# Kernel optimization log

Measured on AMD Instinct MI355X. Metric: run time of the kernel, lower is better.

Reference implementation:

```python
import jax, jax.numpy as jnp
import numpy as np

D_MODEL = 1024
N_HEADS = 16
HEAD_DIM = D_MODEL // N_HEADS
B, S = 2, 2048


def setup_inputs() -> dict:
    key = jax.random.key(0)
    ks = jax.random.split(key, 6)
    w_scale = 1.0 / np.sqrt(D_MODEL)
    return {
        "query": jax.random.normal(ks[0], (B, S, D_MODEL), dtype=jnp.float32),
        "Wq": jax.random.normal(ks[1], (D_MODEL, D_MODEL), dtype=jnp.float32) * w_scale,
        "Wk": jax.random.normal(ks[2], (D_MODEL, D_MODEL), dtype=jnp.float32) * w_scale,
        "Wv": jax.random.normal(ks[3], (D_MODEL, D_MODEL), dtype=jnp.float32) * w_scale,
        "Wo": jax.random.normal(ks[4], (D_MODEL, D_MODEL), dtype=jnp.float32) * w_scale,
        "bo": jnp.zeros((D_MODEL,), dtype=jnp.float32),
    }


def reference(query, Wq, Wk, Wv, Wo, bo):
    # Self-attention: key = value = query (forward() defaults).
    b, t, _ = query.shape
    # Q/K/V projections (nn.Linear applies x @ W.T; weights here are stored as
    # [out, in] like torch, so project with W.T). Split into heads: [B,H,T,Dh].
    def proj(x, W):
        return (x @ W.T).reshape(b, t, N_HEADS, HEAD_DIM).transpose(0, 2, 1, 3)

    q = proj(query, Wq)
    k = proj(query, Wk)
    v = proj(query, Wv)

    scale = 1.0 / np.sqrt(HEAD_DIM)
    scores = jnp.einsum("bhqd,bhkd->bhqk", q, k) * scale  # [B,H,T,T]
    # Causal mask (is_causal=True, not cross-attention).
    causal = jnp.tril(jnp.ones((t, t), dtype=bool))
    scores = jnp.where(causal, scores, jnp.finfo(scores.dtype).min)
    weights = jax.nn.softmax(scores, axis=-1)
    out = jnp.einsum("bhqk,bhkd->bhqd", weights, v)  # [B,H,T,Dh]
    out = out.transpose(0, 2, 1, 3).reshape(b, t, D_MODEL)
    # Output projection with bias (dropout is identity in eval mode).
    return out @ Wo.T + bo
```

## Files before the change

kernel.cpp:

```cpp
#include <hip/hip_runtime.h>
#include <hip/hip_bf16.h>
#include <math.h>

typedef __attribute__((ext_vector_type(8))) short short8;
typedef __attribute__((ext_vector_type(4))) float floatx4;
typedef __attribute__((ext_vector_type(2))) _Float16 half2v;
typedef __attribute__((ext_vector_type(4))) _Float16 half4v;

#define MFMA_BF16_32(a, b, c) __builtin_amdgcn_mfma_f32_16x16x32_bf16(a, b, c, 0, 0, 0)
#define MFMA_F16_16(a, b, c) __builtin_amdgcn_mfma_f32_16x16x16f16(a, b, c, 0, 0, 0)

#define PIPE_BAR2() asm volatile("s_waitcnt vmcnt(2)\n\ts_barrier" ::: "memory")
#define PIPE_BAR0() asm volatile("s_waitcnt vmcnt(0)\n\ts_barrier" ::: "memory")
#define GEMM_BAR4() asm volatile("s_waitcnt vmcnt(4) lgkmcnt(0)\n\ts_barrier" ::: "memory")
#define GEMM_BAR2() asm volatile("s_waitcnt vmcnt(2) lgkmcnt(0)\n\ts_barrier" ::: "memory")
#define GEMM_BAR0() asm volatile("s_waitcnt vmcnt(0) lgkmcnt(0)\n\ts_barrier" ::: "memory")

static constexpr int NH = 16;
static constexpr int Bb = 2;
static constexpr int Ss = 2048;
static constexpr int DM = 1024;

__device__ inline unsigned short f2bf(float f) {
    unsigned int u = __float_as_uint(f);
    u += 0x7fffu + ((u >> 16) & 1u);
    return (unsigned short)(u >> 16);
}

__device__ __forceinline__ half2v pkrtz(float a, float b) {
    return __builtin_bit_cast(half2v, __builtin_amdgcn_cvt_pkrtz(a, b));
}

__device__ __forceinline__ float fexp2(float x) {
#if __has_builtin(__builtin_amdgcn_exp2f)
    return __builtin_amdgcn_exp2f(x);
#else
    return exp2f(x);
#endif
}

__device__ __forceinline__ void gload_lds16(const unsigned short* g, unsigned short* l) {
    __builtin_amdgcn_global_load_lds(
        (const __attribute__((address_space(1))) unsigned int*)g,
        (__attribute__((address_space(3))) unsigned int*)l, 16, 0, 0);
}

__global__ void convert_all(const float* __restrict__ X, const float* __restrict__ w0,
                            const float* __restrict__ w1, const float* __restrict__ w2,
                            const float* __restrict__ w3, unsigned short* __restrict__ dstX,
                            unsigned short* __restrict__ dstW) {
    const int bid = blockIdx.x;
    const float* src;
    unsigned short* dst;
    int i;
    if (bid < 4096) {
        src = X; dst = dstX; i = bid * 256 + threadIdx.x;
    } else {
        const int w = (bid - 4096) >> 10;
        src = (w == 0) ? w0 : (w == 1) ? w1 : (w == 2) ? w2 : w3;
        dst = dstW + (size_t)w * 1048576;
        i = ((bid - 4096) & 1023) * 256 + threadIdx.x;
    }
    float4 v = ((const float4*)src)[i];
    ushort4 o;
    o.x = f2bf(v.x); o.y = f2bf(v.y); o.z = f2bf(v.z); o.w = f2bf(v.w);
    ((ushort4*)dst)[i] = o;
}

__global__ __launch_bounds__(256, 3) void gemm_qkv(const unsigned short* __restrict__ A,
                                                   const unsigned short* __restrict__ W,
                                                   unsigned short* __restrict__ Qp,
                                                   unsigned short* __restrict__ Kp,
                                                   unsigned short* __restrict__ Vt) {
    __shared__ __align__(16) unsigned short S[3][8192];
    const int K = 1024;
    const int tid = threadIdx.x;
    const int wave = tid >> 6, lane = tid & 63;
    const int quad = lane >> 4, l16 = lane & 15;
    const int wr = wave >> 1, wc = wave & 1;

    const int lin = blockIdx.x;
    const int xcd = lin & 7, slot = lin >> 3;
    const int bxt = (xcd & 3) * 8 + (slot & 7);
    const int by = (xcd >> 2) * 12 + (slot >> 3);
    const int bm = bxt * 128;
    const int bn = by * 128;

    const int srow = tid >> 2;
    const int scg = (tid & 3) ^ ((srow >> 1) & 3);
    const unsigned short* gA0 = A + (size_t)(bm + srow) * K + scg * 8;
    const unsigned short* gB0 = W + (size_t)(bn + srow) * K + scg * 8;

    auto stage = [&](int k0, int buf) {
        gload_lds16(gA0 + k0, &S[buf][wave * 512]);
        gload_lds16(gA0 + (size_t)64 * K + k0, &S[buf][2048 + wave * 512]);
        gload_lds16(gB0 + k0, &S[buf][4096 + wave * 512]);
        gload_lds16(gB0 + (size_t)64 * K + k0, &S[buf][6144 + wave * 512]);
    };

    floatx4 acc[4][4];
#pragma unroll
    for (int i = 0; i < 4; i++)
#pragma unroll
        for (int j = 0; j < 4; j++) acc[i][j] = (floatx4)0.0f;

    stage(0, 0);
    stage(32, 1);
    int buf = 0;
    for (int k0 = 0; k0 < K; k0 += 32) {
        if (k0 + 32 < K) { GEMM_BAR4(); } else { GEMM_BAR0(); }
        const int nbuf = (buf == 2) ? 0 : buf + 1;
        const int pbuf = (nbuf == 2) ? 0 : nbuf + 1;
        if (k0 + 64 < K) stage(k0 + 64, pbuf);
        short8 af[4];
#pragma unroll
        for (int im = 0; im < 4; im++) {
            const int frow = wr * 64 + im * 16 + l16;
            af[im] = *(const short8*)&S[buf][frow * 32 + ((quad ^ ((frow >> 1) & 3)) * 8)];
        }
#pragma unroll
        for (int jn = 0; jn < 4; jn++) {
            const int frow = wc * 64 + jn * 16 + l16;
            short8 bf = *(const short8*)&S[buf][4096 + frow * 32 +
                                               ((quad ^ ((frow >> 1) & 3)) * 8)];
#pragma unroll
            for (int im = 0; im < 4; im++) acc[im][jn] = MFMA_BF16_32(af[im], bf, acc[im][jn]);
        }
        buf = nbuf;
    }
    __syncthreads();

    if (by < 16) {
        unsigned short* LB = &S[0][0];
        unsigned short* dst = (by < 8) ? Qp : Kp;
        const int nb = (by & 7) * 128;
        const float scale = (by < 8) ? 0.18033688f : 1.0f;
#pragma unroll
        for (int im = 0; im < 4; im++)
#pragma unroll
            for (int jn = 0; jn < 4; jn++) {
                const int row = wr * 64 + im * 16 + quad * 4;
                const int col = wc * 64 + jn * 16 + l16;
#pragma unroll
                for (int r = 0; r < 4; r++)
                    LB[(row + r) * 132 + col] = f2bf(acc[im][jn][r] * scale);
            }
        __syncthreads();
#pragma unroll
        for (int i = 0; i < 8; ++i) {
            const int flat = i * 256 + tid;
            const int row = flat >> 4, ch = flat & 15;
            short8 v = *(const short8*)&LB[row * 132 + ch * 8];
            *(short8*)&dst[(size_t)(bm + row) * 1024 + nb + ch * 8] = v;
        }
    } else {
        _Float16* LF = (_Float16*)&S[0][0];
        const int dbase = (by - 16) * 128;
        const int bI = bm >> 11, sbase = bm & 2047;
#pragma unroll
        for (int im = 0; im < 4; im++)
#pragma unroll
            for (int jn = 0; jn < 4; jn++) {
                const int d = wc * 64 + jn * 16 + l16;
                const int sl = wr * 64 + im * 16 + quad * 4;
                *(half2v*)&LF[d * 130 + sl] = pkrtz(acc[im][jn][0], acc[im][jn][1]);
                *(half2v*)&LF[d * 130 + sl + 2] = pkrtz(acc[im][jn][2], acc[im][jn][3]);
            }
        __syncthreads();
#pragma unroll
        for (int i = 0; i < 8; ++i) {
            const int flat = i * 256 + tid;
            const int dr = flat >> 4, ch = flat & 15;
            short8 v = *(const short8*)&LF[dr * 130 + ch * 8];
            const int d = dbase + dr;
            const int head = d >> 6, d64 = d & 63;
            *(short8*)&Vt[(((size_t)(bI * 16 + head)) * 64 + d64) * 2048 + sbase + ch * 8] = v;
        }
    }
}

__global__ __launch_bounds__(256, 4) void gemm_out(const unsigned short* __restrict__ A,
                                                   const unsigned short* __restrict__ Bm,
                                                   float* __restrict__ C,
                                                   const float* __restrict__ bias) {
    __shared__ __align__(16) unsigned short As[3][2048];
    __shared__ __align__(16) unsigned short Bs[3][2048];
    const int K = 1024;
    const int tid = threadIdx.x;
    const int wave = tid >> 6, lane = tid & 63;
    const int quad = lane >> 4, l16 = lane & 15;
    const int wr = wave >> 1, wc = wave & 1;

    const int l = blockIdx.x;
    const int xcd = l & 7, slot = l >> 3;
    const int bx = (xcd & 3) * 16 + (slot & 15);
    const int by = (xcd >> 2) * 8 + (slot >> 4);
    const int bm = bx * 64, bn = by * 64;

    const int srow = tid >> 2;
    const int scg = (tid & 3) ^ ((srow >> 1) & 3);
    const unsigned short* gA0 = A + (size_t)(bm + srow) * K + scg * 8;
    const unsigned short* gB0 = Bm + (size_t)(bn + srow) * K + scg * 8;

    auto stage = [&](int k0, int buf) {
        gload_lds16(gA0 + k0, &As[buf][wave * 512]);
        gload_lds16(gB0 + k0, &Bs[buf][wave * 512]);
    };

    floatx4 acc[2][2];
#pragma unroll
    for (int i = 0; i < 2; i++)
#pragma unroll
        for (int j = 0; j < 2; j++) acc[i][j] = (floatx4)0.0f;

    stage(0, 0);
    stage(32, 1);
    int buf = 0;
    for (int k0 = 0; k0 < K; k0 += 32) {
        if (k0 + 32 < K) { GEMM_BAR2(); } else { GEMM_BAR0(); }
        const int nbuf = (buf == 2) ? 0 : buf + 1;
        const int pbuf = (nbuf == 2) ? 0 : nbuf + 1;
        if (k0 + 64 < K) stage(k0 + 64, pbuf);
        short8 af[2];
#pragma unroll
        for (int im = 0; im < 2; im++) {
            const int frow = wr * 32 + im * 16 + l16;
            af[im] = *(const short8*)&As[buf][frow * 32 + ((quad ^ ((frow >> 1) & 3)) * 8)];
        }
#pragma unroll
        for (int jn = 0; jn < 2; jn++) {
            const int frow = wc * 32 + jn * 16 + l16;
            short8 bf = *(const short8*)&Bs[buf][frow * 32 + ((quad ^ ((frow >> 1) & 3)) * 8)];
#pragma unroll
            for (int im = 0; im < 2; im++) acc[im][jn] = MFMA_BF16_32(af[im], bf, acc[im][jn]);
        }
        buf = nbuf;
    }

#pragma unroll
    for (int im = 0; im < 2; im++) {
#pragma unroll
        for (int jn = 0; jn < 2; jn++) {
            const int row0 = bm + wr * 32 + im * 16 + quad * 4;
            const int colg = bn + wc * 32 + jn * 16 + l16;
            const float bv = bias[colg];
#pragma unroll
            for (int r = 0; r < 4; r++)
                C[(size_t)(row0 + r) * 1024 + colg] = acc[im][jn][r] + bv;
        }
    }
}

__global__ __launch_bounds__(512, 4) void flash_attn(const unsigned short* __restrict__ Qp,
                                                     const unsigned short* __restrict__ Kp,
                                                     const _Float16* __restrict__ Vt,
                                                     unsigned short* __restrict__ Out) {
    __shared__ __align__(16) unsigned short Ks[3][4096];
    __shared__ __align__(16) _Float16 Vs[3][4096];
    const int lin = blockIdx.x;
    const int xcd = lin & 7, slot = lin >> 3;
    const int pair = xcd * 4 + ((slot >> 4) & 3);
    const int h = pair & 15, b = pair >> 4;
    const int qt0 = slot & 15;
    const int qt = ((slot >> 5) & 1) ? 15 - qt0 : qt0;

    const int tid = threadIdx.x, w = tid >> 6, lane = tid & 63;
    const int quad = lane >> 4, l16 = lane & 15;

    short8 qf[2];
    {
        const unsigned short* qa =
            Qp + ((size_t)(b * 2048 + qt * 128 + w * 16 + l16) << 10) + h * 64 + quad * 8;
        qf[0] = *(const short8*)qa;
        qf[1] = *(const short8*)(qa + 32);
    }

    const int t8 = tid >> 3;
    const int cg = (tid & 7) ^ (t8 & 7);
    const unsigned short* gK0 = Kp + ((size_t)(b * 2048 + t8) << 10) + h * 64 + cg * 8;
    const _Float16* gV0 = Vt + ((size_t)((b * 16 + h) * 64 + t8) << 11) + cg * 8;
    unsigned short* ldsK = &Ks[0][0] + w * 512;
    _Float16* ldsV = &Vs[0][0] + w * 512;

    auto stage = [&](int kt, int buf) {
        const size_t ko = (size_t)kt << 16;
        const size_t vo = (size_t)kt << 6;
        gload_lds16(gK0 + ko, ldsK + buf * 4096);
        gload_lds16((const unsigned short*)(gV0 + vo), (unsigned short*)(ldsV + buf * 4096));
    };

    const int ktEnd = 2 * qt + 1;
    const int myEnd = 2 * qt + (w >> 2);
    stage(0, 0);
    stage(1, 1);

    floatx4 acc[4];
#pragma unroll
    for (int dt = 0; dt < 4; dt++) acc[dt] = (floatx4)0.0f;
    floatx4 accL = (floatx4)0.0f;
    half4v ones4;
    ones4[0] = ones4[1] = ones4[2] = ones4[3] = (_Float16)1.0f;
    const int qloc = (w & 3) * 16 + l16;
    const int sw = l16 & 7;

    int buf = 0;
    for (int kt = 0; kt <= ktEnd; ++kt) {
        if (kt < ktEnd) { PIPE_BAR2(); } else { PIPE_BAR0(); }
        const int nbuf = (buf == 2) ? 0 : buf + 1;
        const int pbuf = (nbuf == 2) ? 0 : nbuf + 1;
        if (kt + 2 <= ktEnd) stage(kt + 2, pbuf);
        if (kt <= myEnd) {
            const bool diag = (kt == myEnd);
            const int scMax = diag ? (w & 3) : 3;
            const unsigned short* KB = &Ks[buf][0];
            const _Float16* VB = &Vs[buf][0];

#pragma unroll
            for (int sc = 0; sc < 4; ++sc) {
                if (sc <= scMax) {
                    const int rowk = sc * 16 + l16;
                    short8 kf0 = *(const short8*)&KB[rowk * 64 + ((quad ^ sw) * 8)];
                    short8 kf1 = *(const short8*)&KB[rowk * 64 + (((4 + quad) ^ sw) * 8)];

                    floatx4 s = MFMA_BF16_32(kf0, qf[0], (floatx4)(-2.88539008f));
                    s = MFMA_BF16_32(kf1, qf[1], s);
                    float ps[4];
#pragma unroll
                    for (int r = 0; r < 4; ++r) {
                        float e = fexp2(s[r]);
                        if (diag && (sc * 16 + quad * 4 + r > qloc)) e = 0.0f;
                        ps[r] = e;
                    }
                    half4v p = __builtin_shufflevector(pkrtz(ps[0], ps[1]),
                                                       pkrtz(ps[2], ps[3]), 0, 1, 2, 3);
                    accL = MFMA_F16_16(ones4, p, accL);

#pragma unroll
                    for (int dt = 0; dt < 4; ++dt) {
                        const int rowv = dt * 16 + l16;
                        const int cgv = ((sc * 2 + (quad >> 1)) ^ sw);
                        half4v vf = *(const half4v*)&VB[rowv * 64 + cgv * 8 + (quad & 1) * 4];
                        acc[dt] = MFMA_F16_16(vf, p, acc[dt]);
                    }
                }
            }
        }
        buf = nbuf;
    }

    const float inv = 1.0f / accL[0];

    const size_t row = (size_t)(b * 2048 + qt * 128 + w * 16 + l16);
#pragma unroll
    for (int dt = 0; dt < 4; ++dt) {
        const int col = h * 64 + dt * 16 + quad * 4;
        ushort4 o;
        o.x = f2bf(acc[dt][0] * inv);
        o.y = f2bf(acc[dt][1] * inv);
        o.z = f2bf(acc[dt][2] * inv);
        o.w = f2bf(acc[dt][3] * inv);
        *(ushort4*)&Out[row * 1024 + col] = o;
    }
}

extern "C" void kernel_launch(void* const* d_in, const int* in_sizes, int n_in,
                              void* d_out, int out_size, void* d_ws, size_t ws_size,
                              hipStream_t stream) {
    const float* X  = (const float*)d_in[0];
    const float* Wq = (const float*)d_in[1];
    const float* Wk = (const float*)d_in[2];
    const float* Wv = (const float*)d_in[3];
    const float* Wo = (const float*)d_in[4];
    const float* bo = (const float*)d_in[5];

    unsigned short* ws = (unsigned short*)d_ws;
    unsigned short* Xb   = ws;
    unsigned short* W4   = ws + (size_t)4194304;
    unsigned short* Wob  = W4 + (size_t)3145728;
    unsigned short* Qp   = ws + (size_t)8388608;
    unsigned short* Kp   = ws + (size_t)12582912;
    unsigned short* Vt   = ws + (size_t)16777216;
    unsigned short* At   = ws + (size_t)20971520;

    convert_all<<<8192, 256, 0, stream>>>(X, Wq, Wk, Wv, Wo, Xb, W4);

    gemm_qkv<<<768, 256, 0, stream>>>(Xb, W4, Qp, Kp, Vt);

    flash_attn<<<512, 512, 0, stream>>>(Qp, Kp, (const _Float16*)Vt, At);

    gemm_out<<<1024, 256, 0, stream>>>(At, Wob, (float*)d_out, bo);
}
```

Before: 178.4 us.

## Split causal flash attention KV range in two halves and merge partials

Each query tile's key range is split into two halves processed by separate blocks, doubling the attention grid to 1024 blocks. Each half writes unnormalized bf16 partial outputs plus per-row softmax denominators into reused workspace regions. A new merge kernel then sums the two partials and normalizes. The aim is more parallelism and a shorter critical path for long causal tiles. The cost is an extra kernel launch, extra global traffic for the partials, and extra bf16 rounding of the unnormalized sums.

After: 177.0 us. About the same (-0.8%).

```diff
diff --git a/kernel.cpp b/kernel.cpp
--- a/kernel.cpp
+++ b/kernel.cpp
@@ -25,6 +25,10 @@
     unsigned int u = __float_as_uint(f);
     u += 0x7fffu + ((u >> 16) & 1u);
     return (unsigned short)(u >> 16);
+}
+
+__device__ __forceinline__ float bf2f(unsigned short u) {
+    return __uint_as_float((unsigned int)u << 16);
 }
 
 __device__ __forceinline__ half2v pkrtz(float a, float b) {
@@ -254,15 +258,21 @@
 __global__ __launch_bounds__(512, 4) void flash_attn(const unsigned short* __restrict__ Qp,
                                                      const unsigned short* __restrict__ Kp,
                                                      const _Float16* __restrict__ Vt,
-                                                     unsigned short* __restrict__ Out) {
+                                                     unsigned short* __restrict__ P0,
+                                                     unsigned short* __restrict__ P1,
+                                                     float* __restrict__ L0,
+                                                     float* __restrict__ L1) {
     __shared__ __align__(16) unsigned short Ks[3][4096];
     __shared__ __align__(16) _Float16 Vs[3][4096];
     const int lin = blockIdx.x;
     const int xcd = lin & 7, slot = lin >> 3;
-    const int pair = xcd * 4 + ((slot >> 4) & 3);
+    const int g = slot >> 5;
+    const int c = slot & 31;
+    const int pair = xcd * 4 + g;
     const int h = pair & 15, b = pair >> 4;
-    const int qt0 = slot & 15;
-    const int qt = ((slot >> 5) & 1) ? 15 - qt0 : qt0;
+    const int qt0 = c & 15, hf0 = c >> 4;
+    const int qt = (g & 1) ? 15 - qt0 : qt0;
+    const int hf = (g & 2) ? 1 - hf0 : hf0;
 
     const int tid = threadIdx.x, w = tid >> 6, lane = tid & 63;
     const int quad = lane >> 4, l16 = lane & 15;
@@ -289,10 +299,11 @@
         gload_lds16((const unsigned short*)(gV0 + vo), (unsigned short*)(ldsV + buf * 4096));
     };
 
-    const int ktEnd = 2 * qt + 1;
+    const int steps = qt + 1;
+    const int ktA = hf * steps;
     const int myEnd = 2 * qt + (w >> 2);
-    stage(0, 0);
-    stage(1, 1);
+    stage(ktA, 0);
+    if (steps > 1) stage(ktA + 1, 1);
 
     floatx4 acc[4];
 #pragma unroll
@@ -304,11 +315,12 @@
     const int sw = l16 & 7;
 
     int buf = 0;
-    for (int kt = 0; kt <= ktEnd; ++kt) {
-        if (kt < ktEnd) { PIPE_BAR2(); } else { PIPE_BAR0(); }
+    for (int t = 0; t < steps; ++t) {
+        const int kt = ktA + t;
+        if (t + 1 < steps) { PIPE_BAR2(); } else { PIPE_BAR0(); }
         const int nbuf = (buf == 2) ? 0 : buf + 1;
         const int pbuf = (nbuf == 2) ? 0 : nbuf + 1;
-        if (kt + 2 <= ktEnd) stage(kt + 2, pbuf);
+        if (t + 2 < steps) stage(ktA + t + 2, pbuf);
         if (kt <= myEnd) {
             const bool diag = (kt == myEnd);
             const int scMax = diag ? (w & 3) : 3;
@@ -348,19 +360,49 @@
         buf = nbuf;
     }
 
-    const float inv = 1.0f / accL[0];
-
+    unsigned short* P = hf ? P1 : P0;
     const size_t row = (size_t)(b * 2048 + qt * 128 + w * 16 + l16);
 #pragma unroll
     for (int dt = 0; dt < 4; ++dt) {
         const int col = h * 64 + dt * 16 + quad * 4;
         ushort4 o;
-        o.x = f2bf(acc[dt][0] * inv);
-        o.y = f2bf(acc[dt][1] * inv);
-        o.z = f2bf(acc[dt][2] * inv);
-        o.w = f2bf(acc[dt][3] * inv);
-        *(ushort4*)&Out[row * 1024 + col] = o;
-    }
+        o.x = f2bf(acc[dt][0]);
+        o.y = f2bf(acc[dt][1]);
+        o.z = f2bf(acc[dt][2]);
+        o.w = f2bf(acc[dt][3]);
+        *(ushort4*)&P[row * 1024 + col] = o;
+    }
+    if (quad == 0) {
+        float* L = hf ? L1 : L0;
+        L[row * 16 + h] = accL[0];
+    }
+}
+
+__global__ void flash_merge(const unsigned short* __restrict__ P0,
+                            const float* __restrict__ L0,
+                            const float* __restrict__ L1,
+                            unsigned short* __restrict__ At) {
+    const int idx = blockIdx.x * 256 + threadIdx.x;
+    const int row = idx >> 7;
+    const int col0 = (idx & 127) * 8;
+    const int hh = col0 >> 6;
+    const float inv = 1.0f / (L0[row * 16 + hh] + L1[row * 16 + hh]);
+    const size_t off = (size_t)row * 1024 + col0;
+    ushort4 a0 = *(const ushort4*)&P0[off];
+    ushort4 a1 = *(const ushort4*)&P0[off + 4];
+    ushort4 b0 = *(const ushort4*)&At[off];
+    ushort4 b1 = *(const ushort4*)&At[off + 4];
+    ushort4 o0, o1;
+    o0.x = f2bf((bf2f(a0.x) + bf2f(b0.x)) * inv);
+    o0.y = f2bf((bf2f(a0.y) + bf2f(b0.y)) * inv);
+    o0.z = f2bf((bf2f(a0.z) + bf2f(b0.z)) * inv);
+    o0.w = f2bf((bf2f(a0.w) + bf2f(b0.w)) * inv);
+    o1.x = f2bf((bf2f(a1.x) + bf2f(b1.x)) * inv);
+    o1.y = f2bf((bf2f(a1.y) + bf2f(b1.y)) * inv);
+    o1.z = f2bf((bf2f(a1.z) + bf2f(b1.z)) * inv);
+    o1.w = f2bf((bf2f(a1.w) + bf2f(b1.w)) * inv);
+    *(ushort4*)&At[off] = o0;
+    *(ushort4*)&At[off + 4] = o1;
 }
 
 extern "C" void kernel_launch(void* const* d_in, const int* in_sizes, int n_in,
@@ -382,11 +424,19 @@
     unsigned short* Vt   = ws + (size_t)16777216;
     unsigned short* At   = ws + (size_t)20971520;
 
+    unsigned short* Ph0 = Xb;
+    unsigned short* Ph1 = At;
+    float* L0 = (float*)(ws + (size_t)4194304);
+    float* L1 = L0 + 65536;
+
     convert_all<<<8192, 256, 0, stream>>>(X, Wq, Wk, Wv, Wo, Xb, W4);
 
     gemm_qkv<<<768, 256, 0, stream>>>(Xb, W4, Qp, Kp, Vt);
 
-    flash_attn<<<512, 512, 0, stream>>>(Qp, Kp, (const _Float16*)Vt, At);
+    flash_attn<<<1024, 512, 0, stream>>>(Qp, Kp, (const _Float16*)Vt,
+                                         Ph0, Ph1, L0, L1);
+
+    flash_merge<<<2048, 256, 0, stream>>>(Ph0, L0, L1, At);
 
     gemm_out<<<1024, 256, 0, stream>>>(At, Wob, (float*)d_out, bo);
 }
```
